# Performance work log

Hardware: AMD Instinct MI355X
Metric: run time of the kernel (lower is better)

Reference implementation:

```python
import math
import jax, jax.numpy as jnp
import numpy as np

LOG_2PI = math.log(2.0 * math.pi)


def setup_inputs() -> dict:
    key = jax.random.key(0)
    k1, k2, k3 = jax.random.split(key, 3)
    B, C, H, W = 64, 3, 32, 32
    N = 50000
    x = jax.random.normal(k1, (B, C, H, W), dtype=jnp.float32)
    # positive noise levels in [0.1, 2.0)
    sigma = jax.random.uniform(k2, (B,), dtype=jnp.float32) * 1.9 + 0.1
    Y = jax.random.normal(k3, (N, C, H, W), dtype=jnp.float32)
    return {"x": x, "sigma": sigma, "Y": Y}


def reference(x, sigma, Y):
    # x: [B,C,H,W], sigma: [B], Y: [N,C,H,W]
    B = x.shape[0]
    N = Y.shape[0]
    D = x.shape[1] * x.shape[2] * x.shape[3]  # dims summed in _log_normal_prob
    xf = x.reshape(B, D)
    Yf = Y.reshape(N, D)
    x2 = jnp.sum(xf * xf, axis=1, keepdims=True)          # [B,1]
    y2 = jnp.sum(Yf * Yf, axis=1)[None, :]                # [1,N]
    d2 = jnp.maximum(x2 + y2 - 2.0 * (xf @ Yf.T), 0.0)    # [B,N]
    inv_var = 1.0 / (sigma * sigma)                        # [B]
    # sum_d log N(x_d; y_d, sigma^2) = -0.5*d2/sigma^2 - D*log(sigma) - 0.5*D*log(2pi)
    log_p = (-0.5 * d2 * inv_var[:, None]
             - D * jnp.log(sigma)[:, None]
             - 0.5 * D * LOG_2PI)                          # [B,N]
    # softmax over the train set == exp(log_p - logsumexp(log_p))
    w = jax.nn.softmax(log_p, axis=1)                      # [B,N]
    out = (w @ Yf).reshape(x.shape)                        # weighted average of train images
    return out
```

## Files before the change

kernel.cpp:

```cpp
#include <hip/hip_runtime.h>


#define BB 64
#define DD 3072
#define NN 50000
#define NSPAD 50176
#define NGRP 384
#define SGRP 6272
#define NCHK 896

typedef __attribute__((ext_vector_type(8))) short bf16x8;
typedef __attribute__((ext_vector_type(4))) float f32x4;

__device__ __forceinline__ unsigned short f2bf(float f) {
  unsigned u = __float_as_uint(f);
  u += 0x7FFFu + ((u >> 16) & 1u);
  return (unsigned short)(u >> 16);
}
__device__ __forceinline__ float bf2f(unsigned short h) {
  return __uint_as_float(((unsigned)h) << 16);
}

__global__ __launch_bounds__(256) void xpose_kernel(const float* __restrict__ x,
                                                    const float* __restrict__ sigma,
                                                    unsigned short* __restrict__ XhiP,
                                                    unsigned short* __restrict__ XloP,
                                                    float* __restrict__ x2g,
                                                    float* __restrict__ ivg) {
  const int b = blockIdx.x;
  const int t = threadIdx.x;
  const float4* xr = (const float4*)(x + (long)b * DD);
  float ss = 0.f;
#pragma unroll
  for (int i = 0; i < 3; ++i) {
    int idx = t + i * 256;
    float4 v = xr[idx];
    int grp = idx >> 1;
    int off = (idx & 1) * 4;
    ushort4 hh, ll;
    hh.x = f2bf(v.x); ll.x = f2bf(v.x - bf2f(hh.x));
    hh.y = f2bf(v.y); ll.y = f2bf(v.y - bf2f(hh.y));
    hh.z = f2bf(v.z); ll.z = f2bf(v.z - bf2f(hh.z));
    hh.w = f2bf(v.w); ll.w = f2bf(v.w - bf2f(hh.w));
    long o = ((long)grp * 64 + b) * 8 + off;
    *(ushort4*)(XhiP + o) = hh;
    *(ushort4*)(XloP + o) = ll;
    ss = fmaf(v.x, v.x, ss); ss = fmaf(v.y, v.y, ss);
    ss = fmaf(v.z, v.z, ss); ss = fmaf(v.w, v.w, ss);
  }
#pragma unroll
  for (int off = 32; off > 0; off >>= 1) ss += __shfl_down(ss, off, 64);
  __shared__ float red[4];
  if ((t & 63) == 0) red[t >> 6] = ss;
  __syncthreads();
  if (t == 0) {
    x2g[b] = red[0] + red[1] + red[2] + red[3];
    float sg = sigma[b];
    ivg[b] = 1.f / (sg * sg);
  }
}

__global__ __launch_bounds__(256) void score_kernel(const float* __restrict__ Y,
                                                    const unsigned short* __restrict__ XhiP,
                                                    const unsigned short* __restrict__ XloP,
                                                    const float* __restrict__ x2g,
                                                    const float* __restrict__ ivg,
                                                    float* __restrict__ sT) {
  const int t = threadIdx.x;
  const int w = t >> 6;
  const int l = t & 63;
  const int l15 = l & 15, q = l >> 4;
  const int n = blockIdx.x * 64 + w * 16 + l15;
  const long nc = (n < NN) ? n : (NN - 1);
  const float* yrow = Y + nc * (long)DD + q * 8;

  __shared__ float x2s[64], ivs[64];
  __shared__ float tr[4][16][68];
  if (t < 64) { x2s[t] = x2g[t]; ivs[t] = ivg[t]; }
  __syncthreads();

  f32x4 acc[4] = {};
  float y2 = 0.f;

  for (int kt = 0; kt < DD; kt += 32) {
    float4 b0 = *(const float4*)(yrow + kt);
    float4 b1 = *(const float4*)(yrow + kt + 4);
    const int grp = (kt >> 3) + q;
    const bf16x8* Ah = (const bf16x8*)XhiP + (long)grp * 64 + l15;
    const bf16x8* Al = (const bf16x8*)XloP + (long)grp * 64 + l15;
    bf16x8 a_h[4], a_l[4];
#pragma unroll
    for (int mt = 0; mt < 4; ++mt) { a_h[mt] = Ah[mt * 16]; a_l[mt] = Al[mt * 16]; }

    y2 = fmaf(b0.x, b0.x, y2); y2 = fmaf(b0.y, b0.y, y2);
    y2 = fmaf(b0.z, b0.z, y2); y2 = fmaf(b0.w, b0.w, y2);
    y2 = fmaf(b1.x, b1.x, y2); y2 = fmaf(b1.y, b1.y, y2);
    y2 = fmaf(b1.z, b1.z, y2); y2 = fmaf(b1.w, b1.w, y2);

    float fv[8] = {b0.x, b0.y, b0.z, b0.w, b1.x, b1.y, b1.z, b1.w};
    bf16x8 bh, bl;
#pragma unroll
    for (int j = 0; j < 8; ++j) {
      unsigned short h = f2bf(fv[j]);
      bh[j] = (short)h;
      bl[j] = (short)f2bf(fv[j] - bf2f(h));
    }
#pragma unroll
    for (int mt = 0; mt < 4; ++mt) {
      acc[mt] = __builtin_amdgcn_mfma_f32_16x16x32_bf16(a_h[mt], bh, acc[mt], 0, 0, 0);
      acc[mt] = __builtin_amdgcn_mfma_f32_16x16x32_bf16(a_h[mt], bl, acc[mt], 0, 0, 0);
      acc[mt] = __builtin_amdgcn_mfma_f32_16x16x32_bf16(a_l[mt], bh, acc[mt], 0, 0, 0);
    }
  }

  y2 += __shfl_xor(y2, 16, 64);
  y2 += __shfl_xor(y2, 32, 64);

#pragma unroll
  for (int mt = 0; mt < 4; ++mt) {
#pragma unroll
    for (int r = 0; r < 4; ++r) {
      int b = mt * 16 + q * 4 + r;
      float s = fminf(-0.5f * ivs[b] * (x2s[b] + y2 - 2.f * acc[mt][r]), 0.f);
      tr[w][l15][b] = s;
    }
  }
  __syncthreads();
  const long nrow = (long)blockIdx.x * 64 + w * 16 + l15;
  float* dst = sT + nrow * 64 + q * 16;
  const float* src = &tr[w][l15][q * 16];
  *(float4*)(dst + 0)  = *(const float4*)(src + 0);
  *(float4*)(dst + 4)  = *(const float4*)(src + 4);
  *(float4*)(dst + 8)  = *(const float4*)(src + 8);
  *(float4*)(dst + 12) = *(const float4*)(src + 12);
}

__global__ __launch_bounds__(256) void softstat1_kernel(const float* __restrict__ sT,
                                                        float* __restrict__ pM,
                                                        float* __restrict__ pL) {
  const int t = threadIdx.x;
  const int b = t & 63;
  const int g = t >> 6;
  const int slot = blockIdx.x * 4 + g;
  float m[4], l[4];
#pragma unroll
  for (int u = 0; u < 4; ++u) { m[u] = -3.402823466e38f; l[u] = 0.f; }
  for (int j = 0; j < 52; j += 4) {
    float sv[4];
#pragma unroll
    for (int u = 0; u < 4; ++u) {
      int n = slot + (j + u) * 1024;
      sv[u] = (n < NN) ? sT[(long)n * 64 + b] : -3.402823466e38f;
    }
#pragma unroll
    for (int u = 0; u < 4; ++u) {
      float nm = fmaxf(m[u], sv[u]);
      l[u] = fmaf(l[u], __expf(m[u] - nm), __expf(sv[u] - nm));
      m[u] = nm;
    }
  }
#pragma unroll
  for (int u = 1; u < 4; ++u) {
    float nm = fmaxf(m[0], m[u]);
    l[0] = fmaf(l[0], __expf(m[0] - nm), l[u] * __expf(m[u] - nm));
    m[0] = nm;
  }
  __shared__ float sm[256], sl[256];
  sm[t] = m[0]; sl[t] = l[0];
  __syncthreads();
  if (g == 0) {
    float mm = m[0], ll = l[0];
#pragma unroll
    for (int j = 1; j < 4; ++j) {
      float m2 = sm[j * 64 + b], l2 = sl[j * 64 + b];
      float nm = fmaxf(mm, m2);
      ll = fmaf(ll, __expf(mm - nm), l2 * __expf(m2 - nm));
      mm = nm;
    }
    pM[blockIdx.x * 64 + b] = mm;
    pL[blockIdx.x * 64 + b] = ll;
  }
}

__global__ __launch_bounds__(256) void softstat2_kernel(const float* __restrict__ pM,
                                                        const float* __restrict__ pL,
                                                        float* __restrict__ mg,
                                                        float* __restrict__ rlg) {
  const int t = threadIdx.x;
  const int b = t & 63;
  const int g = t >> 6;
  float m = -3.402823466e38f, l = 0.f;
  for (int i = g; i < 256; i += 4) {
    float m2 = pM[i * 64 + b], l2 = pL[i * 64 + b];
    float nm = fmaxf(m, m2);
    l = fmaf(l, __expf(m - nm), l2 * __expf(m2 - nm));
    m = nm;
  }
  __shared__ float sm[256], sl[256];
  sm[t] = m; sl[t] = l;
  __syncthreads();
  if (g == 0) {
#pragma unroll
    for (int j = 1; j < 4; ++j) {
      float m2 = sm[j * 64 + b], l2 = sl[j * 64 + b];
      float nm = fmaxf(m, m2);
      l = fmaf(l, __expf(m - nm), l2 * __expf(m2 - nm));
      m = nm;
    }
    mg[b] = m;
    rlg[b] = 1.f / l;
  }
}

__global__ __launch_bounds__(256) void wprep_kernel(const float* __restrict__ sT,
                                                    const float* __restrict__ mg,
                                                    const float* __restrict__ rlg,
                                                    unsigned short* __restrict__ WH,
                                                    unsigned short* __restrict__ WL) {
  const int t = threadIdx.x;
  const int b = t & 63;
  const int grp = blockIdx.x * 4 + (t >> 6);
  const float mb = mg[b], rb = rlg[b];
  bf16x8 H, L;
#pragma unroll
  for (int j = 0; j < 8; ++j) {
    int n = grp * 8 + j;
    float s = sT[(long)n * 64 + b];
    float wv = (n < NN) ? __expf(s - mb) * rb : 0.f;
    unsigned short h = f2bf(wv);
    H[j] = (short)h;
    L[j] = (short)f2bf(wv - bf2f(h));
  }
  *((bf16x8*)WH + (long)grp * 64 + b) = H;
  *((bf16x8*)WL + (long)grp * 64 + b) = L;
}

__global__ __launch_bounds__(256) void wsum_kernel(const float* __restrict__ Y,
                                                   const unsigned short* __restrict__ WH,
                                                   const unsigned short* __restrict__ WL,
                                                   float* __restrict__ out) {
  const int t = threadIdx.x;
  const int w = t >> 6;
  const int l = t & 63;
  const int l15 = l & 15, q = l >> 4;
  const int dblk = blockIdx.x % 24;
  const int c = blockIdx.x / 24;
  const int d0 = dblk * 128 + w * 32 + l15;
  const int nstart = c * NCHK;

  f32x4 acc[4][2] = {};

  for (int k0 = nstart; k0 < nstart + NCHK; k0 += 32) {
    const int grp = (k0 >> 3) + q;
    const bf16x8* Ah = (const bf16x8*)WH + (long)grp * 64 + l15;
    const bf16x8* Al = (const bf16x8*)WL + (long)grp * 64 + l15;
    bf16x8 wh[4], wl[4];
#pragma unroll
    for (int mt = 0; mt < 4; ++mt) { wh[mt] = Ah[mt * 16]; wl[mt] = Al[mt * 16]; }

    const int rbase = k0 + q * 8;
    float f0[8], f1[8];
#pragma unroll
    for (int j = 0; j < 8; ++j) {
      long r = rbase + j;
      r = (r < NN) ? r : (NN - 1);
      const float* yp = Y + r * (long)DD + d0;
      f0[j] = yp[0];
      f1[j] = yp[16];
    }
    bf16x8 yh0, yl0, yh1, yl1;
#pragma unroll
    for (int j = 0; j < 8; ++j) {
      unsigned short h0 = f2bf(f0[j]);
      yh0[j] = (short)h0; yl0[j] = (short)f2bf(f0[j] - bf2f(h0));
      unsigned short h1 = f2bf(f1[j]);
      yh1[j] = (short)h1; yl1[j] = (short)f2bf(f1[j] - bf2f(h1));
    }
#pragma unroll
    for (int mt = 0; mt < 4; ++mt) {
      acc[mt][0] = __builtin_amdgcn_mfma_f32_16x16x32_bf16(wh[mt], yh0, acc[mt][0], 0, 0, 0);
      acc[mt][0] = __builtin_amdgcn_mfma_f32_16x16x32_bf16(wh[mt], yl0, acc[mt][0], 0, 0, 0);
      acc[mt][0] = __builtin_amdgcn_mfma_f32_16x16x32_bf16(wl[mt], yh0, acc[mt][0], 0, 0, 0);
      acc[mt][1] = __builtin_amdgcn_mfma_f32_16x16x32_bf16(wh[mt], yh1, acc[mt][1], 0, 0, 0);
      acc[mt][1] = __builtin_amdgcn_mfma_f32_16x16x32_bf16(wh[mt], yl1, acc[mt][1], 0, 0, 0);
      acc[mt][1] = __builtin_amdgcn_mfma_f32_16x16x32_bf16(wl[mt], yh1, acc[mt][1], 0, 0, 0);
    }
  }

#pragma unroll
  for (int mt = 0; mt < 4; ++mt)
#pragma unroll
    for (int dt = 0; dt < 2; ++dt)
#pragma unroll
      for (int r = 0; r < 4; ++r) {
        int b = mt * 16 + q * 4 + r;
        unsafeAtomicAdd(&out[(long)b * DD + d0 + dt * 16], acc[mt][dt][r]);
      }
}

extern "C" void kernel_launch(void* const* d_in, const int* in_sizes, int n_in,
                              void* d_out, int out_size, void* d_ws, size_t ws_size,
                              hipStream_t stream) {
  const float* x = (const float*)d_in[0];
  const float* sigma = (const float*)d_in[1];
  const float* Y = (const float*)d_in[2];
  float* out = (float*)d_out;

  char* p = (char*)d_ws;
  float* sT = (float*)p;            p += (long)NSPAD * 64 * 4;
  unsigned short* WH = (unsigned short*)p; p += (long)NSPAD * 64 * 2;
  unsigned short* WL = (unsigned short*)p; p += (long)NSPAD * 64 * 2;
  unsigned short* XhiP = (unsigned short*)p; p += (long)NGRP * 64 * 8 * 2;
  unsigned short* XloP = (unsigned short*)p; p += (long)NGRP * 64 * 8 * 2;
  float* x2g = (float*)p; p += 64 * 4;
  float* ivg = (float*)p; p += 64 * 4;
  float* mg  = (float*)p; p += 64 * 4;
  float* rlg = (float*)p; p += 64 * 4;
  float* pM  = (float*)p; p += 256 * 64 * 4;
  float* pL  = (float*)p; p += 256 * 64 * 4;

  hipMemsetAsync(d_out, 0, (size_t)out_size * sizeof(float), stream);
  hipLaunchKernelGGL(xpose_kernel, dim3(BB), dim3(256), 0, stream,
                     x, sigma, XhiP, XloP, x2g, ivg);
  hipLaunchKernelGGL(score_kernel, dim3(782), dim3(256), 0, stream,
                     Y, XhiP, XloP, x2g, ivg, sT);
  hipLaunchKernelGGL(softstat1_kernel, dim3(256), dim3(256), 0, stream, sT, pM, pL);
  hipLaunchKernelGGL(softstat2_kernel, dim3(1), dim3(256), 0, stream, pM, pL, mg, rlg);
  hipLaunchKernelGGL(wprep_kernel, dim3(SGRP / 4), dim3(256), 0, stream,
                     sT, mg, rlg, WH, WL);
  hipLaunchKernelGGL(wsum_kernel, dim3(24 * 56), dim3(256), 0, stream,
                     Y, WH, WL, out);
}
```

Before: 1.133 ms.

## Fuse per-block softmax statistics into score kernel and halve block size

The score kernel now computes per-block running max and sum-of-exp for each query using wave shuffles and writes partials directly, which removes the separate softstat1 pass that re-read the whole score matrix. The score blocks shrink from 256 to 128 threads, giving 1563 blocks for better CU balance, and the final reduction kernel grows to 1024 threads to merge the larger number of partials. The bf16 conversion also switches to the HIP intrinsic. The fused reduction adds shuffle and exp work to the score kernel's epilogue.

```diff
diff --git a/kernel.cpp b/kernel.cpp
--- a/kernel.cpp
+++ b/kernel.cpp
@@ -1,4 +1,5 @@
 #include <hip/hip_runtime.h>
+#include <hip/hip_bf16.h>
 
 
 #define BB 64
@@ -8,14 +9,14 @@
 #define NGRP 384
 #define SGRP 6272
 #define NCHK 896
+#define SBLK 1563
 
 typedef __attribute__((ext_vector_type(8))) short bf16x8;
 typedef __attribute__((ext_vector_type(4))) float f32x4;
 
 __device__ __forceinline__ unsigned short f2bf(float f) {
-  unsigned u = __float_as_uint(f);
-  u += 0x7FFFu + ((u >> 16) & 1u);
-  return (unsigned short)(u >> 16);
+  __hip_bfloat16 h = __float2bfloat16(f);
+  return __builtin_bit_cast(unsigned short, h);
 }
 __device__ __forceinline__ float bf2f(unsigned short h) {
   return __uint_as_float(((unsigned)h) << 16);
@@ -60,22 +61,25 @@
   }
 }
 
-__global__ __launch_bounds__(256) void score_kernel(const float* __restrict__ Y,
+__global__ __launch_bounds__(128) void score_kernel(const float* __restrict__ Y,
                                                     const unsigned short* __restrict__ XhiP,
                                                     const unsigned short* __restrict__ XloP,
                                                     const float* __restrict__ x2g,
                                                     const float* __restrict__ ivg,
-                                                    float* __restrict__ sT) {
+                                                    float* __restrict__ sT,
+                                                    float* __restrict__ pM,
+                                                    float* __restrict__ pL) {
   const int t = threadIdx.x;
   const int w = t >> 6;
   const int l = t & 63;
   const int l15 = l & 15, q = l >> 4;
-  const int n = blockIdx.x * 64 + w * 16 + l15;
+  const int n = blockIdx.x * 32 + w * 16 + l15;
   const long nc = (n < NN) ? n : (NN - 1);
   const float* yrow = Y + nc * (long)DD + q * 8;
 
   __shared__ float x2s[64], ivs[64];
-  __shared__ float tr[4][16][68];
+  __shared__ float tr[2][16][68];
+  __shared__ float swm[2][64], swl[2][64];
   if (t < 64) { x2s[t] = x2g[t]; ivs[t] = ivg[t]; }
   __syncthreads();
 
@@ -116,92 +120,82 @@
   y2 += __shfl_xor(y2, 16, 64);
   y2 += __shfl_xor(y2, 32, 64);
 
+  float sv[4][4];
 #pragma unroll
   for (int mt = 0; mt < 4; ++mt) {
 #pragma unroll
     for (int r = 0; r < 4; ++r) {
       int b = mt * 16 + q * 4 + r;
       float s = fminf(-0.5f * ivs[b] * (x2s[b] + y2 - 2.f * acc[mt][r]), 0.f);
+      sv[mt][r] = s;
       tr[w][l15][b] = s;
     }
   }
+
+  const bool valid = (n < NN);
+  const float NEG = -3.402823466e38f;
+#pragma unroll
+  for (int mt = 0; mt < 4; ++mt) {
+#pragma unroll
+    for (int r = 0; r < 4; ++r) {
+      float s = valid ? sv[mt][r] : NEG;
+      float sm = s;
+      sm = fmaxf(sm, __shfl_xor(sm, 1, 64));
+      sm = fmaxf(sm, __shfl_xor(sm, 2, 64));
+      sm = fmaxf(sm, __shfl_xor(sm, 4, 64));
+      sm = fmaxf(sm, __shfl_xor(sm, 8, 64));
+      float e = valid ? __expf(sv[mt][r] - sm) : 0.f;
+      e += __shfl_xor(e, 1, 64);
+      e += __shfl_xor(e, 2, 64);
+      e += __shfl_xor(e, 4, 64);
+      e += __shfl_xor(e, 8, 64);
+      if (l15 == 0) {
+        int b = mt * 16 + q * 4 + r;
+        swm[w][b] = sm;
+        swl[w][b] = e;
+      }
+    }
+  }
   __syncthreads();
-  const long nrow = (long)blockIdx.x * 64 + w * 16 + l15;
+
+  const long nrow = (long)blockIdx.x * 32 + w * 16 + l15;
   float* dst = sT + nrow * 64 + q * 16;
   const float* src = &tr[w][l15][q * 16];
   *(float4*)(dst + 0)  = *(const float4*)(src + 0);
   *(float4*)(dst + 4)  = *(const float4*)(src + 4);
   *(float4*)(dst + 8)  = *(const float4*)(src + 8);
   *(float4*)(dst + 12) = *(const float4*)(src + 12);
-}
-
-__global__ __launch_bounds__(256) void softstat1_kernel(const float* __restrict__ sT,
-                                                        float* __restrict__ pM,
-                                                        float* __restrict__ pL) {
-  const int t = threadIdx.x;
-  const int b = t & 63;
-  const int g = t >> 6;
-  const int slot = blockIdx.x * 4 + g;
-  float m[4], l[4];
-#pragma unroll
-  for (int u = 0; u < 4; ++u) { m[u] = -3.402823466e38f; l[u] = 0.f; }
-  for (int j = 0; j < 52; j += 4) {
-    float sv[4];
-#pragma unroll
-    for (int u = 0; u < 4; ++u) {
-      int n = slot + (j + u) * 1024;
-      sv[u] = (n < NN) ? sT[(long)n * 64 + b] : -3.402823466e38f;
-    }
-#pragma unroll
-    for (int u = 0; u < 4; ++u) {
-      float nm = fmaxf(m[u], sv[u]);
-      l[u] = fmaf(l[u], __expf(m[u] - nm), __expf(sv[u] - nm));
-      m[u] = nm;
-    }
-  }
-#pragma unroll
-  for (int u = 1; u < 4; ++u) {
-    float nm = fmaxf(m[0], m[u]);
-    l[0] = fmaf(l[0], __expf(m[0] - nm), l[u] * __expf(m[u] - nm));
-    m[0] = nm;
-  }
-  __shared__ float sm[256], sl[256];
-  sm[t] = m[0]; sl[t] = l[0];
-  __syncthreads();
-  if (g == 0) {
-    float mm = m[0], ll = l[0];
-#pragma unroll
-    for (int j = 1; j < 4; ++j) {
-      float m2 = sm[j * 64 + b], l2 = sl[j * 64 + b];
-      float nm = fmaxf(mm, m2);
-      ll = fmaf(ll, __expf(mm - nm), l2 * __expf(m2 - nm));
-      mm = nm;
-    }
-    pM[blockIdx.x * 64 + b] = mm;
-    pL[blockIdx.x * 64 + b] = ll;
-  }
-}
-
-__global__ __launch_bounds__(256) void softstat2_kernel(const float* __restrict__ pM,
-                                                        const float* __restrict__ pL,
-                                                        float* __restrict__ mg,
-                                                        float* __restrict__ rlg) {
+
+  if (t < 64) {
+    float m0 = swm[0][t], l0 = swl[0][t];
+    float m1 = swm[1][t], l1 = swl[1][t];
+    float nm = fmaxf(m0, m1);
+    float ll = l0 * __expf(m0 - nm) + l1 * __expf(m1 - nm);
+    pM[(long)blockIdx.x * 64 + t] = nm;
+    pL[(long)blockIdx.x * 64 + t] = ll;
+  }
+}
+
+__global__ __launch_bounds__(1024) void softstat2_kernel(const float* __restrict__ pM,
+                                                         const float* __restrict__ pL,
+                                                         float* __restrict__ mg,
+                                                         float* __restrict__ rlg) {
   const int t = threadIdx.x;
   const int b = t & 63;
   const int g = t >> 6;
   float m = -3.402823466e38f, l = 0.f;
-  for (int i = g; i < 256; i += 4) {
-    float m2 = pM[i * 64 + b], l2 = pL[i * 64 + b];
+  for (int i = g; i < SBLK; i += 16) {
+    float m2 = pM[(long)i * 64 + b], l2 = pL[(long)i * 64 + b];
     float nm = fmaxf(m, m2);
     l = fmaf(l, __expf(m - nm), l2 * __expf(m2 - nm));
     m = nm;
   }
-  __shared__ float sm[256], sl[256];
+  __shared__ float sm[1024], sl[1024];
   sm[t] = m; sl[t] = l;
   __syncthreads();
   if (g == 0) {
 #pragma unroll
-    for (int j = 1; j < 4; ++j) {
+    for (int j = 1; j < 16; ++j) {
       float m2 = sm[j * 64 + b], l2 = sl[j * 64 + b];
       float nm = fmaxf(m, m2);
       l = fmaf(l, __expf(m - nm), l2 * __expf(m2 - nm));
@@ -316,16 +310,15 @@
   float* ivg = (float*)p; p += 64 * 4;
   float* mg  = (float*)p; p += 64 * 4;
   float* rlg = (float*)p; p += 64 * 4;
-  float* pM  = (float*)p; p += 256 * 64 * 4;
-  float* pL  = (float*)p; p += 256 * 64 * 4;
+  float* pM  = (float*)p; p += (long)SBLK * 64 * 4;
+  float* pL  = (float*)p; p += (long)SBLK * 64 * 4;
 
   hipMemsetAsync(d_out, 0, (size_t)out_size * sizeof(float), stream);
   hipLaunchKernelGGL(xpose_kernel, dim3(BB), dim3(256), 0, stream,
                      x, sigma, XhiP, XloP, x2g, ivg);
-  hipLaunchKernelGGL(score_kernel, dim3(782), dim3(256), 0, stream,
-                     Y, XhiP, XloP, x2g, ivg, sT);
-  hipLaunchKernelGGL(softstat1_kernel, dim3(256), dim3(256), 0, stream, sT, pM, pL);
-  hipLaunchKernelGGL(softstat2_kernel, dim3(1), dim3(256), 0, stream, pM, pL, mg, rlg);
+  hipLaunchKernelGGL(score_kernel, dim3(SBLK), dim3(128), 0, stream,
+                     Y, XhiP, XloP, x2g, ivg, sT, pM, pL);
+  hipLaunchKernelGGL(softstat2_kernel, dim3(1), dim3(1024), 0, stream, pM, pL, mg, rlg);
   hipLaunchKernelGGL(wprep_kernel, dim3(SGRP / 4), dim3(256), 0, stream,
                      sT, mg, rlg, WH, WL);
   hipLaunchKernelGGL(wsum_kernel, dim3(24 * 56), dim3(256), 0, stream,
```

Result: no change. 1.118 ms (-1.3%).
